# Optimization experiments

Measured on AMD Instinct MI355X. Metric: run time of the kernel, lower is better.

The kernel has to match this reference:

```python
import jax, jax.numpy as jnp
import numpy as np

B, S, H, E, K, D = 1, 4096, 1024, 8, 2, 2048

def setup_inputs() -> dict:
    key = jax.random.key(0)
    k1, k2, k3, k4, k5 = jax.random.split(key, 5)
    x = jax.random.normal(k1, (B, S, H), dtype=jnp.float32)
    attention_mask = jnp.ones((B, S), dtype=jnp.int32)
    expert_weights = jax.random.uniform(k2, (B, S, K), dtype=jnp.float32)
    # distinct top-K expert indices per token (torch code requires at most one match per token)
    r = jax.random.uniform(k3, (B, S, E))
    chosen_expert_indices = jnp.argsort(r, axis=-1)[..., :K].astype(jnp.int64)
    down_proj = jax.random.normal(k4, (E, H, D), dtype=jnp.float32)
    up_proj = jax.random.normal(k5, (E, D, H), dtype=jnp.float32)
    return {"x": x, "attention_mask": attention_mask, "expert_weights": expert_weights,
            "chosen_expert_indices": chosen_expert_indices, "down_proj": down_proj, "up_proj": up_proj}

def reference(x, attention_mask, expert_weights, chosen_expert_indices, down_proj, up_proj):
    b, s, h = x.shape
    e = down_proj.shape[0]
    xt = x.reshape(-1, h)                                   # [N,H]
    n = xt.shape[0]
    mask = attention_mask.reshape(n, 1).astype(x.dtype)     # [N,1]
    idx = chosen_expert_indices.reshape(n, -1)              # [N,K]
    w = expert_weights.reshape(n, -1)                       # [N,K]
    onehot = jax.nn.one_hot(idx, e, dtype=x.dtype)          # [N,K,E]
    # per-token routing weight for each expert (0 if not chosen), masked
    we = jnp.einsum('nk,nke->ne', w, onehot) * mask         # [N,E]
    hid = jax.nn.relu(jnp.einsum('nh,ehd->end', xt, down_proj))  # [E,N,D]
    y = jnp.einsum('end,edh->enh', hid, up_proj)            # [E,N,H]
    mlp = jnp.einsum('ne,enh->nh', we, y)                   # [N,H]
    out = xt + mlp                                          # residual (B==1 as in source)
    return out.reshape(b, s, h)
```

## Files before the change

### kernel.cpp

```cpp
#include <hip/hip_runtime.h>
#include <stdint.h>

#define NTOK 4096
#define HDIM 1024
#define DDIM 2048
#define NEXP 8
#define NASS 8192

typedef __attribute__((ext_vector_type(8))) short bf16x8;
typedef __attribute__((ext_vector_type(4))) float f32x4;

typedef __attribute__((address_space(1))) const unsigned int gu32;
typedef __attribute__((address_space(3))) unsigned int lu32;

#define BARRIER() asm volatile("s_barrier" ::: "memory")
#define WAIT_VM0() asm volatile("s_waitcnt vmcnt(0)" ::: "memory")
#define WAIT_LGKM0() do { asm volatile("s_waitcnt lgkmcnt(0)" ::: "memory"); \
                          __builtin_amdgcn_sched_barrier(0); } while (0)

__device__ __forceinline__ void async16(void* lds, const void* g) {
  __builtin_amdgcn_global_load_lds((gu32*)(uintptr_t)g, (lu32*)(uintptr_t)lds, 16, 0, 0);
}

__device__ __forceinline__ unsigned short f2bf(float f) {
  unsigned int u = __float_as_uint(f);
  return (unsigned short)((u + 0x7fffu + ((u >> 16) & 1u)) >> 16);
}
__device__ __forceinline__ float bf2f(unsigned short u) {
  return __uint_as_float(((unsigned int)u) << 16);
}

__global__ __launch_bounds__(256) void k_cvt_x(const float* __restrict__ x,
                                               unsigned short* __restrict__ x16) {
  int i = blockIdx.x * 256 + threadIdx.x;
  float4 v = reinterpret_cast<const float4*>(x)[i];
  ushort4 o;
  o.x = f2bf(v.x); o.y = f2bf(v.y); o.z = f2bf(v.z); o.w = f2bf(v.w);
  reinterpret_cast<ushort4*>(x16)[i] = o;
}

__global__ __launch_bounds__(256) void k_transpose(const float* __restrict__ in,
                                                   unsigned short* __restrict__ out,
                                                   int R, int C) {
  __shared__ float t[32][33];
  const size_t mbase = (size_t)blockIdx.z * R * C;
  int tid = threadIdx.x;
  int r = tid >> 3, c4 = (tid & 7) * 4;
  int gr = blockIdx.y * 32 + r;
  int gc = blockIdx.x * 32 + c4;
  float4 v = *reinterpret_cast<const float4*>(in + mbase + (size_t)gr * C + gc);
  t[r][c4 + 0] = v.x; t[r][c4 + 1] = v.y; t[r][c4 + 2] = v.z; t[r][c4 + 3] = v.w;
  __syncthreads();
  int orow = blockIdx.x * 32 + r;
  int oc4  = blockIdx.y * 32 + c4;
  ushort4 o;
  o.x = f2bf(t[c4 + 0][r]); o.y = f2bf(t[c4 + 1][r]);
  o.z = f2bf(t[c4 + 2][r]); o.w = f2bf(t[c4 + 3][r]);
  *reinterpret_cast<ushort4*>(out + mbase + (size_t)orow * R + oc4) = o;
}

__global__ __launch_bounds__(1024) void k_route(
    const int* __restrict__ idx, const float* __restrict__ ew,
    const int* __restrict__ amask,
    int* __restrict__ counts_g, int* __restrict__ offs_g,
    int* __restrict__ toks, float* __restrict__ wl, int* __restrict__ slotmap) {
  __shared__ int cnt[NEXP], cur[NEXP], flag;
  const int t = threadIdx.x;
  if (t < NEXP) cnt[t] = 0;
  if (t == 0) flag = 0;
  __syncthreads();
  int lf = 0;
#pragma unroll
  for (int j = 0; j < 4; ++j) {
    int i = t + j * 1024;
    if (idx[2 * i + 1] != 0) lf = 1;
  }
  if (lf) atomicOr(&flag, 1);
  __syncthreads();
  const int is32 = flag;
  int e[8];
#pragma unroll
  for (int j = 0; j < 8; ++j) {
    int i = t + j * 1024;
    int ei = is32 ? idx[i] : idx[2 * i];
    e[j] = ei;
    atomicAdd(&cnt[ei], 1);
  }
  __syncthreads();
  if (t == 0) {
    int off = 0;
    for (int k = 0; k < NEXP; ++k) {
      cur[k] = off; offs_g[k] = off; counts_g[k] = cnt[k]; off += cnt[k];
    }
  }
  __syncthreads();
#pragma unroll
  for (int j = 0; j < 8; ++j) {
    int i = t + j * 1024;
    int n = i >> 1;
    int slot = atomicAdd(&cur[e[j]], 1);
    toks[slot] = n;
    wl[slot] = ew[i] * (amask[n] ? 1.0f : 0.0f);
    slotmap[i] = slot;
  }
}

__global__ __launch_bounds__(512, 2) void k_gemm_down(
    const unsigned short* __restrict__ x16, const unsigned short* __restrict__ bT,
    const int* __restrict__ counts, const int* __restrict__ offs,
    const int* __restrict__ toks, unsigned short* __restrict__ hid) {
  const int e = blockIdx.x;
  const int cnt = counts[e];
  const int q = blockIdx.y;
  const int mt = q >> 3;
  const int nt = q & 7;
  if (mt * 256 >= cnt) return;
  const int base = offs[e];
  __shared__ alignas(16) char lds[131072];
  const int tid = threadIdx.x;
  const int lane = tid & 63;
  const int wr = ((tid >> 8) & 1) * 128;
  const int wc = ((tid >> 6) & 3) * 64;

  const char* gA[4]; const char* gB[4]; int sOff[4];
  {
    const int swcol = ((tid & 7) << 4) ^ (((tid >> 3) & 7) << 4);
#pragma unroll
    for (int s = 0; s < 4; ++s) {
      int row = s * 64 + (tid >> 3);
      int sl = mt * 256 + row; if (sl >= cnt) sl = cnt - 1;
      gA[s] = (const char*)(x16 + (size_t)toks[base + sl] * HDIM) + swcol;
      gB[s] = (const char*)(bT + (size_t)e * DDIM * HDIM + (size_t)(nt * 256 + row) * HDIM) + swcol;
      sOff[s] = s * 8192 + tid * 16;
    }
  }
  const int swz = (lane & 7) << 4;
  const int lo = (lane >> 4) << 4;
  int rowA[8], rowB[4];
#pragma unroll
  for (int m = 0; m < 8; ++m) rowA[m] = (wr + m * 16 + (lane & 15)) * 128;
#pragma unroll
  for (int n = 0; n < 4; ++n) rowB[n] = (wc + n * 16 + (lane & 15)) * 128;

#pragma unroll
  for (int s = 0; s < 4; ++s) {
    async16(lds + sOff[s], gA[s]);
    async16(lds + 65536 + sOff[s], gB[s]);
  }

  f32x4 acc[8][4] = {};
  for (int j = 0; j < 16; ++j) {
    WAIT_VM0();
    BARRIER();
    char* curA = lds + ((j & 1) << 15);
    char* curB = lds + 65536 + ((j & 1) << 15);
    if (j < 15) {
      const int ko = (j + 1) << 7;
      char* nA = lds + ((~j & 1) << 15);
      char* nB = lds + 65536 + ((~j & 1) << 15);
#pragma unroll
      for (int s = 0; s < 4; ++s) {
        async16(nA + sOff[s], gA[s] + ko);
        async16(nB + sOff[s], gB[s] + ko);
      }
    }
#pragma unroll
    for (int ks = 0; ks < 2; ++ks) {
      const int cx = ((ks << 6) | lo) ^ swz;
      bf16x8 fa[8], fb[4];
#pragma unroll
      for (int n = 0; n < 4; ++n) fb[n] = *reinterpret_cast<const bf16x8*>(curB + rowB[n] + cx);
#pragma unroll
      for (int m = 0; m < 8; ++m) fa[m] = *reinterpret_cast<const bf16x8*>(curA + rowA[m] + cx);
      WAIT_LGKM0();
      __builtin_amdgcn_s_setprio(1);
#pragma unroll
      for (int m = 0; m < 8; ++m)
#pragma unroll
        for (int n = 0; n < 4; ++n)
          acc[m][n] = __builtin_amdgcn_mfma_f32_16x16x32_bf16(fa[m], fb[n], acc[m][n], 0, 0, 0);
      __builtin_amdgcn_s_setprio(0);
    }
  }

#pragma unroll
  for (int m = 0; m < 8; ++m) {
    int r0 = mt * 256 + wr + m * 16 + ((lane >> 4) * 4);
#pragma unroll
    for (int jj = 0; jj < 4; ++jj) {
      int r = r0 + jj;
      if (r < cnt) {
        unsigned short* dst = hid + (size_t)(base + r) * DDIM + nt * 256 + wc + (lane & 15);
#pragma unroll
        for (int n = 0; n < 4; ++n) {
          float v = acc[m][n][jj];
          dst[n * 16] = f2bf(v > 0.f ? v : 0.f);
        }
      }
    }
  }
}

__global__ __launch_bounds__(512, 2) void k_gemm_up(
    const unsigned short* __restrict__ hid, const unsigned short* __restrict__ bT,
    const int* __restrict__ counts, const int* __restrict__ offs,
    unsigned short* __restrict__ yw) {
  const int e = blockIdx.x;
  const int cnt = counts[e];
  const int q = blockIdx.y;
  const int nt = q & 3;
  const int mt = (q >> 2) & 15;
  const int ksp = q >> 6;
  if (mt * 256 >= cnt) return;
  const int base = offs[e];
  __shared__ alignas(16) char lds[131072];
  const int tid = threadIdx.x;
  const int lane = tid & 63;
  const int wr = ((tid >> 8) & 1) * 128;
  const int wc = ((tid >> 6) & 3) * 64;

  const char* gA[4]; const char* gB[4]; int sOff[4];
  {
    const int swcol = ((tid & 7) << 4) ^ (((tid >> 3) & 7) << 4);
#pragma unroll
    for (int s = 0; s < 4; ++s) {
      int row = s * 64 + (tid >> 3);
      int sl = mt * 256 + row; if (sl >= cnt) sl = cnt - 1;
      gA[s] = (const char*)(hid + (size_t)(base + sl) * DDIM + ksp * 1024) + swcol;
      gB[s] = (const char*)(bT + (size_t)e * HDIM * DDIM + (size_t)(nt * 256 + row) * DDIM + ksp * 1024) + swcol;
      sOff[s] = s * 8192 + tid * 16;
    }
  }
  const int swz = (lane & 7) << 4;
  const int lo = (lane >> 4) << 4;
  int rowA[8], rowB[4];
#pragma unroll
  for (int m = 0; m < 8; ++m) rowA[m] = (wr + m * 16 + (lane & 15)) * 128;
#pragma unroll
  for (int n = 0; n < 4; ++n) rowB[n] = (wc + n * 16 + (lane & 15)) * 128;

#pragma unroll
  for (int s = 0; s < 4; ++s) {
    async16(lds + sOff[s], gA[s]);
    async16(lds + 65536 + sOff[s], gB[s]);
  }

  f32x4 acc[8][4] = {};
  for (int j = 0; j < 16; ++j) {
    WAIT_VM0();
    BARRIER();
    char* curA = lds + ((j & 1) << 15);
    char* curB = lds + 65536 + ((j & 1) << 15);
    if (j < 15) {
      const int ko = (j + 1) << 7;
      char* nA = lds + ((~j & 1) << 15);
      char* nB = lds + 65536 + ((~j & 1) << 15);
#pragma unroll
      for (int s = 0; s < 4; ++s) {
        async16(nA + sOff[s], gA[s] + ko);
        async16(nB + sOff[s], gB[s] + ko);
      }
    }
#pragma unroll
    for (int ks = 0; ks < 2; ++ks) {
      const int cx = ((ks << 6) | lo) ^ swz;
      bf16x8 fa[8], fb[4];
#pragma unroll
      for (int n = 0; n < 4; ++n) fb[n] = *reinterpret_cast<const bf16x8*>(curB + rowB[n] + cx);
#pragma unroll
      for (int m = 0; m < 8; ++m) fa[m] = *reinterpret_cast<const bf16x8*>(curA + rowA[m] + cx);
      WAIT_LGKM0();
      __builtin_amdgcn_s_setprio(1);
#pragma unroll
      for (int m = 0; m < 8; ++m)
#pragma unroll
        for (int n = 0; n < 4; ++n)
          acc[m][n] = __builtin_amdgcn_mfma_f32_16x16x32_bf16(fa[m], fb[n], acc[m][n], 0, 0, 0);
      __builtin_amdgcn_s_setprio(0);
    }
  }

#pragma unroll
  for (int m = 0; m < 8; ++m) {
    int r0 = mt * 256 + wr + m * 16 + ((lane >> 4) * 4);
#pragma unroll
    for (int jj = 0; jj < 4; ++jj) {
      int r = r0 + jj;
      if (r < cnt) {
        unsigned short* dst = yw + ((size_t)ksp * NASS + base + r) * HDIM
                              + nt * 256 + wc + (lane & 15);
#pragma unroll
        for (int n = 0; n < 4; ++n) dst[n * 16] = f2bf(acc[m][n][jj]);
      }
    }
  }
}

__global__ __launch_bounds__(256) void k_combine(
    const float* __restrict__ x, const unsigned short* __restrict__ yw,
    const int* __restrict__ slotmap, const float* __restrict__ wl,
    float* __restrict__ out) {
  const int n = blockIdx.x;
  const int t = threadIdx.x;
  const int s0 = slotmap[2 * n], s1 = slotmap[2 * n + 1];
  const float w0 = wl[s0], w1 = wl[s1];
  float4 xv = reinterpret_cast<const float4*>(x + (size_t)n * HDIM)[t];
  ushort4 a0 = reinterpret_cast<const ushort4*>(yw + (size_t)s0 * HDIM)[t];
  ushort4 a1 = reinterpret_cast<const ushort4*>(yw + ((size_t)NASS + s0) * HDIM)[t];
  ushort4 b0 = reinterpret_cast<const ushort4*>(yw + (size_t)s1 * HDIM)[t];
  ushort4 b1 = reinterpret_cast<const ushort4*>(yw + ((size_t)NASS + s1) * HDIM)[t];
  float4 r;
  r.x = xv.x + w0 * (bf2f(a0.x) + bf2f(a1.x)) + w1 * (bf2f(b0.x) + bf2f(b1.x));
  r.y = xv.y + w0 * (bf2f(a0.y) + bf2f(a1.y)) + w1 * (bf2f(b0.y) + bf2f(b1.y));
  r.z = xv.z + w0 * (bf2f(a0.z) + bf2f(a1.z)) + w1 * (bf2f(b0.z) + bf2f(b1.z));
  r.w = xv.w + w0 * (bf2f(a0.w) + bf2f(a1.w)) + w1 * (bf2f(b0.w) + bf2f(b1.w));
  reinterpret_cast<float4*>(out + (size_t)n * HDIM)[t] = r;
}

extern "C" void kernel_launch(void* const* d_in, const int* in_sizes, int n_in,
                              void* d_out, int out_size, void* d_ws, size_t ws_size,
                              hipStream_t stream) {
  const float* x    = (const float*)d_in[0];
  const int* amask  = (const int*)d_in[1];
  const float* ew   = (const float*)d_in[2];
  const int* cidx   = (const int*)d_in[3];
  const float* dn   = (const float*)d_in[4];
  const float* up   = (const float*)d_in[5];
  float* out        = (float*)d_out;
  char* ws          = (char*)d_ws;

  const size_t X16_OFF = 0;
  const size_t DNT_OFF = X16_OFF + (size_t)NTOK * HDIM * 2;
  const size_t UPT_OFF = DNT_OFF + (size_t)NEXP * HDIM * DDIM * 2;
  const size_t HID_OFF = UPT_OFF + (size_t)NEXP * HDIM * DDIM * 2;
  const size_t MET_OFF = HID_OFF + (size_t)NASS * DDIM * 2;

  unsigned short* x16 = (unsigned short*)(ws + X16_OFF);
  unsigned short* dnT = (unsigned short*)(ws + DNT_OFF);
  unsigned short* upT = (unsigned short*)(ws + UPT_OFF);
  unsigned short* hid = (unsigned short*)(ws + HID_OFF);
  unsigned short* yw  = (unsigned short*)(ws + DNT_OFF);
  int* counts  = (int*)(ws + MET_OFF);
  int* offs    = counts + 8;
  int* toks    = counts + 32;
  float* wl    = (float*)(toks + NASS);
  int* slotmap = (int*)(wl + NASS);

  k_cvt_x<<<NTOK * HDIM / 1024, 256, 0, stream>>>(x, x16);
  k_transpose<<<dim3(DDIM / 32, HDIM / 32, NEXP), 256, 0, stream>>>(dn, dnT, HDIM, DDIM);
  k_transpose<<<dim3(HDIM / 32, DDIM / 32, NEXP), 256, 0, stream>>>(up, upT, DDIM, HDIM);
  k_route<<<1, 1024, 0, stream>>>(cidx, ew, amask, counts, offs, toks, wl, slotmap);
  k_gemm_down<<<dim3(8, 128), 512, 0, stream>>>(x16, dnT, counts, offs, toks, hid);
  k_gemm_up<<<dim3(8, 128), 512, 0, stream>>>(hid, upT, counts, offs, yw);
  k_combine<<<NTOK, 256, 0, stream>>>(x, yw, slotmap, wl, out);
}
```

Measured before the change: 172.2 us.

## Fuse prep kernels, shrink GEMM tiles to 128x128, drop up-proj split-K

Merges the x conversion and both weight transposes into one prep launch. Both grouped GEMMs go from 256x256 tiles with 512 threads to 128x128 tiles with 256 threads and half the LDS, so more blocks can be resident per CU. The up GEMM no longer splits K into two partial outputs, so the combine step reads one partial per expert instead of two. Smaller tiles lower per-block operand reuse and raise total global traffic for the weights.

```diff
diff --git a/kernel.cpp b/kernel.cpp
--- a/kernel.cpp
+++ b/kernel.cpp
@@ -30,33 +30,50 @@
   return __uint_as_float(((unsigned int)u) << 16);
 }
 
-__global__ __launch_bounds__(256) void k_cvt_x(const float* __restrict__ x,
-                                               unsigned short* __restrict__ x16) {
-  int i = blockIdx.x * 256 + threadIdx.x;
-  float4 v = reinterpret_cast<const float4*>(x)[i];
+__device__ __forceinline__ void transpose_tile(const float* __restrict__ in,
+                                               unsigned short* __restrict__ out,
+                                               int R, int C, int e, int bx, int by,
+                                               float* tb, int tid) {
+  const size_t mbase = (size_t)e * R * C;
+  int r = tid >> 3, c4 = (tid & 7) * 4;
+  int gr = by * 32 + r;
+  int gc = bx * 32 + c4;
+  float4 v = *reinterpret_cast<const float4*>(in + mbase + (size_t)gr * C + gc);
+  tb[r * 33 + c4 + 0] = v.x; tb[r * 33 + c4 + 1] = v.y;
+  tb[r * 33 + c4 + 2] = v.z; tb[r * 33 + c4 + 3] = v.w;
+  __syncthreads();
+  int orow = bx * 32 + r;
+  int oc4  = by * 32 + c4;
   ushort4 o;
-  o.x = f2bf(v.x); o.y = f2bf(v.y); o.z = f2bf(v.z); o.w = f2bf(v.w);
-  reinterpret_cast<ushort4*>(x16)[i] = o;
-}
-
-__global__ __launch_bounds__(256) void k_transpose(const float* __restrict__ in,
-                                                   unsigned short* __restrict__ out,
-                                                   int R, int C) {
-  __shared__ float t[32][33];
-  const size_t mbase = (size_t)blockIdx.z * R * C;
-  int tid = threadIdx.x;
-  int r = tid >> 3, c4 = (tid & 7) * 4;
-  int gr = blockIdx.y * 32 + r;
-  int gc = blockIdx.x * 32 + c4;
-  float4 v = *reinterpret_cast<const float4*>(in + mbase + (size_t)gr * C + gc);
-  t[r][c4 + 0] = v.x; t[r][c4 + 1] = v.y; t[r][c4 + 2] = v.z; t[r][c4 + 3] = v.w;
-  __syncthreads();
-  int orow = blockIdx.x * 32 + r;
-  int oc4  = blockIdx.y * 32 + c4;
-  ushort4 o;
-  o.x = f2bf(t[c4 + 0][r]); o.y = f2bf(t[c4 + 1][r]);
-  o.z = f2bf(t[c4 + 2][r]); o.w = f2bf(t[c4 + 3][r]);
+  o.x = f2bf(tb[(c4 + 0) * 33 + r]); o.y = f2bf(tb[(c4 + 1) * 33 + r]);
+  o.z = f2bf(tb[(c4 + 2) * 33 + r]); o.w = f2bf(tb[(c4 + 3) * 33 + r]);
   *reinterpret_cast<ushort4*>(out + mbase + (size_t)orow * R + oc4) = o;
+}
+
+__global__ __launch_bounds__(256) void k_prep(
+    const float* __restrict__ x, unsigned short* __restrict__ x16,
+    const float* __restrict__ dn, unsigned short* __restrict__ dnT,
+    const float* __restrict__ up, unsigned short* __restrict__ upT) {
+  __shared__ float tb[32 * 33];
+  const int b = blockIdx.x;
+  const int tid = threadIdx.x;
+  if (b < 4096) {
+    int i = b * 256 + tid;
+    float4 v = reinterpret_cast<const float4*>(x)[i];
+    ushort4 o;
+    o.x = f2bf(v.x); o.y = f2bf(v.y); o.z = f2bf(v.z); o.w = f2bf(v.w);
+    reinterpret_cast<ushort4*>(x16)[i] = o;
+  } else if (b < 4096 + 16384) {
+    int idx = b - 4096;
+    int e = idx >> 11, t = idx & 2047;
+    int bx = t & 63, by = t >> 6;
+    transpose_tile(dn, dnT, HDIM, DDIM, e, bx, by, tb, tid);
+  } else {
+    int idx = b - 20480;
+    int e = idx >> 11, t = idx & 2047;
+    int bx = t & 31, by = t >> 5;
+    transpose_tile(up, upT, DDIM, HDIM, e, bx, by, tb, tid);
+  }
 }
 
 __global__ __launch_bounds__(1024) void k_route(
@@ -105,59 +122,59 @@
   }
 }
 
-__global__ __launch_bounds__(512, 2) void k_gemm_down(
+__global__ __launch_bounds__(256, 4) void k_gemm_down(
     const unsigned short* __restrict__ x16, const unsigned short* __restrict__ bT,
     const int* __restrict__ counts, const int* __restrict__ offs,
     const int* __restrict__ toks, unsigned short* __restrict__ hid) {
   const int e = blockIdx.x;
   const int cnt = counts[e];
   const int q = blockIdx.y;
-  const int mt = q >> 3;
-  const int nt = q & 7;
-  if (mt * 256 >= cnt) return;
+  const int mt = q >> 4;
+  const int nt = q & 15;
+  if (mt * 128 >= cnt) return;
   const int base = offs[e];
-  __shared__ alignas(16) char lds[131072];
+  __shared__ alignas(16) char lds[65536];
   const int tid = threadIdx.x;
   const int lane = tid & 63;
-  const int wr = ((tid >> 8) & 1) * 128;
-  const int wc = ((tid >> 6) & 3) * 64;
+  const int wr = ((tid >> 7) & 1) * 64;
+  const int wc = ((tid >> 6) & 1) * 64;
 
   const char* gA[4]; const char* gB[4]; int sOff[4];
   {
     const int swcol = ((tid & 7) << 4) ^ (((tid >> 3) & 7) << 4);
 #pragma unroll
     for (int s = 0; s < 4; ++s) {
-      int row = s * 64 + (tid >> 3);
-      int sl = mt * 256 + row; if (sl >= cnt) sl = cnt - 1;
+      int row = s * 32 + (tid >> 3);
+      int sl = mt * 128 + row; if (sl >= cnt) sl = cnt - 1;
       gA[s] = (const char*)(x16 + (size_t)toks[base + sl] * HDIM) + swcol;
-      gB[s] = (const char*)(bT + (size_t)e * DDIM * HDIM + (size_t)(nt * 256 + row) * HDIM) + swcol;
-      sOff[s] = s * 8192 + tid * 16;
+      gB[s] = (const char*)(bT + (size_t)e * DDIM * HDIM + (size_t)(nt * 128 + row) * HDIM) + swcol;
+      sOff[s] = s * 4096 + tid * 16;
     }
   }
   const int swz = (lane & 7) << 4;
   const int lo = (lane >> 4) << 4;
-  int rowA[8], rowB[4];
-#pragma unroll
-  for (int m = 0; m < 8; ++m) rowA[m] = (wr + m * 16 + (lane & 15)) * 128;
+  int rowA[4], rowB[4];
+#pragma unroll
+  for (int m = 0; m < 4; ++m) rowA[m] = (wr + m * 16 + (lane & 15)) * 128;
 #pragma unroll
   for (int n = 0; n < 4; ++n) rowB[n] = (wc + n * 16 + (lane & 15)) * 128;
 
 #pragma unroll
   for (int s = 0; s < 4; ++s) {
     async16(lds + sOff[s], gA[s]);
-    async16(lds + 65536 + sOff[s], gB[s]);
-  }
-
-  f32x4 acc[8][4] = {};
+    async16(lds + 32768 + sOff[s], gB[s]);
+  }
+
+  f32x4 acc[4][4] = {};
   for (int j = 0; j < 16; ++j) {
     WAIT_VM0();
     BARRIER();
-    char* curA = lds + ((j & 1) << 15);
-    char* curB = lds + 65536 + ((j & 1) << 15);
+    char* curA = lds + ((j & 1) << 14);
+    char* curB = lds + 32768 + ((j & 1) << 14);
     if (j < 15) {
       const int ko = (j + 1) << 7;
-      char* nA = lds + ((~j & 1) << 15);
-      char* nB = lds + 65536 + ((~j & 1) << 15);
+      char* nA = lds + ((~j & 1) << 14);
+      char* nB = lds + 32768 + ((~j & 1) << 14);
 #pragma unroll
       for (int s = 0; s < 4; ++s) {
         async16(nA + sOff[s], gA[s] + ko);
@@ -167,15 +184,15 @@
 #pragma unroll
     for (int ks = 0; ks < 2; ++ks) {
       const int cx = ((ks << 6) | lo) ^ swz;
-      bf16x8 fa[8], fb[4];
+      bf16x8 fa[4], fb[4];
 #pragma unroll
       for (int n = 0; n < 4; ++n) fb[n] = *reinterpret_cast<const bf16x8*>(curB + rowB[n] + cx);
 #pragma unroll
-      for (int m = 0; m < 8; ++m) fa[m] = *reinterpret_cast<const bf16x8*>(curA + rowA[m] + cx);
+      for (int m = 0; m < 4; ++m) fa[m] = *reinterpret_cast<const bf16x8*>(curA + rowA[m] + cx);
       WAIT_LGKM0();
       __builtin_amdgcn_s_setprio(1);
 #pragma unroll
-      for (int m = 0; m < 8; ++m)
+      for (int m = 0; m < 4; ++m)
 #pragma unroll
         for (int n = 0; n < 4; ++n)
           acc[m][n] = __builtin_amdgcn_mfma_f32_16x16x32_bf16(fa[m], fb[n], acc[m][n], 0, 0, 0);
@@ -184,13 +201,13 @@
   }
 
 #pragma unroll
-  for (int m = 0; m < 8; ++m) {
-    int r0 = mt * 256 + wr + m * 16 + ((lane >> 4) * 4);
+  for (int m = 0; m < 4; ++m) {
+    int r0 = mt * 128 + wr + m * 16 + ((lane >> 4) * 4);
 #pragma unroll
     for (int jj = 0; jj < 4; ++jj) {
       int r = r0 + jj;
       if (r < cnt) {
-        unsigned short* dst = hid + (size_t)(base + r) * DDIM + nt * 256 + wc + (lane & 15);
+        unsigned short* dst = hid + (size_t)(base + r) * DDIM + nt * 128 + wc + (lane & 15);
 #pragma unroll
         for (int n = 0; n < 4; ++n) {
           float v = acc[m][n][jj];
@@ -201,60 +218,59 @@
   }
 }
 
-__global__ __launch_bounds__(512, 2) void k_gemm_up(
+__global__ __launch_bounds__(256, 4) void k_gemm_up(
     const unsigned short* __restrict__ hid, const unsigned short* __restrict__ bT,
     const int* __restrict__ counts, const int* __restrict__ offs,
     unsigned short* __restrict__ yw) {
   const int e = blockIdx.x;
   const int cnt = counts[e];
   const int q = blockIdx.y;
-  const int nt = q & 3;
-  const int mt = (q >> 2) & 15;
-  const int ksp = q >> 6;
-  if (mt * 256 >= cnt) return;
+  const int mt = q >> 3;
+  const int nt = q & 7;
+  if (mt * 128 >= cnt) return;
   const int base = offs[e];
-  __shared__ alignas(16) char lds[131072];
+  __shared__ alignas(16) char lds[65536];
   const int tid = threadIdx.x;
   const int lane = tid & 63;
-  const int wr = ((tid >> 8) & 1) * 128;
-  const int wc = ((tid >> 6) & 3) * 64;
+  const int wr = ((tid >> 7) & 1) * 64;
+  const int wc = ((tid >> 6) & 1) * 64;
 
   const char* gA[4]; const char* gB[4]; int sOff[4];
   {
     const int swcol = ((tid & 7) << 4) ^ (((tid >> 3) & 7) << 4);
 #pragma unroll
     for (int s = 0; s < 4; ++s) {
-      int row = s * 64 + (tid >> 3);
-      int sl = mt * 256 + row; if (sl >= cnt) sl = cnt - 1;
-      gA[s] = (const char*)(hid + (size_t)(base + sl) * DDIM + ksp * 1024) + swcol;
-      gB[s] = (const char*)(bT + (size_t)e * HDIM * DDIM + (size_t)(nt * 256 + row) * DDIM + ksp * 1024) + swcol;
-      sOff[s] = s * 8192 + tid * 16;
+      int row = s * 32 + (tid >> 3);
+      int sl = mt * 128 + row; if (sl >= cnt) sl = cnt - 1;
+      gA[s] = (const char*)(hid + (size_t)(base + sl) * DDIM) + swcol;
+      gB[s] = (const char*)(bT + (size_t)e * HDIM * DDIM + (size_t)(nt * 128 + row) * DDIM) + swcol;
+      sOff[s] = s * 4096 + tid * 16;
     }
   }
   const int swz = (lane & 7) << 4;
   const int lo = (lane >> 4) << 4;
-  int rowA[8], rowB[4];
-#pragma unroll
-  for (int m = 0; m < 8; ++m) rowA[m] = (wr + m * 16 + (lane & 15)) * 128;
+  int rowA[4], rowB[4];
+#pragma unroll
+  for (int m = 0; m < 4; ++m) rowA[m] = (wr + m * 16 + (lane & 15)) * 128;
 #pragma unroll
   for (int n = 0; n < 4; ++n) rowB[n] = (wc + n * 16 + (lane & 15)) * 128;
 
 #pragma unroll
   for (int s = 0; s < 4; ++s) {
     async16(lds + sOff[s], gA[s]);
-    async16(lds + 65536 + sOff[s], gB[s]);
-  }
-
-  f32x4 acc[8][4] = {};
-  for (int j = 0; j < 16; ++j) {
+    async16(lds + 32768 + sOff[s], gB[s]);
+  }
+
+  f32x4 acc[4][4] = {};
+  for (int j = 0; j < 32; ++j) {
     WAIT_VM0();
     BARRIER();
-    char* curA = lds + ((j & 1) << 15);
-    char* curB = lds + 65536 + ((j & 1) << 15);
-    if (j < 15) {
+    char* curA = lds + ((j & 1) << 14);
+    char* curB = lds + 32768 + ((j & 1) << 14);
+    if (j < 31) {
       const int ko = (j + 1) << 7;
-      char* nA = lds + ((~j & 1) << 15);
-      char* nB = lds + 65536 + ((~j & 1) << 15);
+      char* nA = lds + ((~j & 1) << 14);
+      char* nB = lds + 32768 + ((~j & 1) << 14);
 #pragma unroll
       for (int s = 0; s < 4; ++s) {
         async16(nA + sOff[s], gA[s] + ko);
@@ -264,15 +280,15 @@
 #pragma unroll
     for (int ks = 0; ks < 2; ++ks) {
       const int cx = ((ks << 6) | lo) ^ swz;
-      bf16x8 fa[8], fb[4];
+      bf16x8 fa[4], fb[4];
 #pragma unroll
       for (int n = 0; n < 4; ++n) fb[n] = *reinterpret_cast<const bf16x8*>(curB + rowB[n] + cx);
 #pragma unroll
-      for (int m = 0; m < 8; ++m) fa[m] = *reinterpret_cast<const bf16x8*>(curA + rowA[m] + cx);
+      for (int m = 0; m < 4; ++m) fa[m] = *reinterpret_cast<const bf16x8*>(curA + rowA[m] + cx);
       WAIT_LGKM0();
       __builtin_amdgcn_s_setprio(1);
 #pragma unroll
-      for (int m = 0; m < 8; ++m)
+      for (int m = 0; m < 4; ++m)
 #pragma unroll
         for (int n = 0; n < 4; ++n)
           acc[m][n] = __builtin_amdgcn_mfma_f32_16x16x32_bf16(fa[m], fb[n], acc[m][n], 0, 0, 0);
@@ -281,14 +297,13 @@
   }
 
 #pragma unroll
-  for (int m = 0; m < 8; ++m) {
-    int r0 = mt * 256 + wr + m * 16 + ((lane >> 4) * 4);
+  for (int m = 0; m < 4; ++m) {
+    int r0 = mt * 128 + wr + m * 16 + ((lane >> 4) * 4);
 #pragma unroll
     for (int jj = 0; jj < 4; ++jj) {
       int r = r0 + jj;
       if (r < cnt) {
-        unsigned short* dst = yw + ((size_t)ksp * NASS + base + r) * HDIM
-                              + nt * 256 + wc + (lane & 15);
+        unsigned short* dst = yw + (size_t)(base + r) * HDIM + nt * 128 + wc + (lane & 15);
 #pragma unroll
         for (int n = 0; n < 4; ++n) dst[n * 16] = f2bf(acc[m][n][jj]);
       }
@@ -306,14 +321,12 @@
   const float w0 = wl[s0], w1 = wl[s1];
   float4 xv = reinterpret_cast<const float4*>(x + (size_t)n * HDIM)[t];
   ushort4 a0 = reinterpret_cast<const ushort4*>(yw + (size_t)s0 * HDIM)[t];
-  ushort4 a1 = reinterpret_cast<const ushort4*>(yw + ((size_t)NASS + s0) * HDIM)[t];
   ushort4 b0 = reinterpret_cast<const ushort4*>(yw + (size_t)s1 * HDIM)[t];
-  ushort4 b1 = reinterpret_cast<const ushort4*>(yw + ((size_t)NASS + s1) * HDIM)[t];
   float4 r;
-  r.x = xv.x + w0 * (bf2f(a0.x) + bf2f(a1.x)) + w1 * (bf2f(b0.x) + bf2f(b1.x));
-  r.y = xv.y + w0 * (bf2f(a0.y) + bf2f(a1.y)) + w1 * (bf2f(b0.y) + bf2f(b1.y));
-  r.z = xv.z + w0 * (bf2f(a0.z) + bf2f(a1.z)) + w1 * (bf2f(b0.z) + bf2f(b1.z));
-  r.w = xv.w + w0 * (bf2f(a0.w) + bf2f(a1.w)) + w1 * (bf2f(b0.w) + bf2f(b1.w));
+  r.x = xv.x + w0 * bf2f(a0.x) + w1 * bf2f(b0.x);
+  r.y = xv.y + w0 * bf2f(a0.y) + w1 * bf2f(b0.y);
+  r.z = xv.z + w0 * bf2f(a0.z) + w1 * bf2f(b0.z);
+  r.w = xv.w + w0 * bf2f(a0.w) + w1 * bf2f(b0.w);
   reinterpret_cast<float4*>(out + (size_t)n * HDIM)[t] = r;
 }
 
@@ -346,11 +359,9 @@
   float* wl    = (float*)(toks + NASS);
   int* slotmap = (int*)(wl + NASS);
 
-  k_cvt_x<<<NTOK * HDIM / 1024, 256, 0, stream>>>(x, x16);
-  k_transpose<<<dim3(DDIM / 32, HDIM / 32, NEXP), 256, 0, stream>>>(dn, dnT, HDIM, DDIM);
-  k_transpose<<<dim3(HDIM / 32, DDIM / 32, NEXP), 256, 0, stream>>>(up, upT, DDIM, HDIM);
+  k_prep<<<4096 + 16384 + 16384, 256, 0, stream>>>(x, x16, dn, dnT, up, upT);
   k_route<<<1, 1024, 0, stream>>>(cidx, ew, amask, counts, offs, toks, wl, slotmap);
-  k_gemm_down<<<dim3(8, 128), 512, 0, stream>>>(x16, dnT, counts, offs, toks, hid);
-  k_gemm_up<<<dim3(8, 128), 512, 0, stream>>>(hid, upT, counts, offs, yw);
+  k_gemm_down<<<dim3(8, 1024), 256, 0, stream>>>(x16, dnT, counts, offs, toks, hid);
+  k_gemm_up<<<dim3(8, 512), 256, 0, stream>>>(hid, upT, counts, offs, yw);
   k_combine<<<NTOK, 256, 0, stream>>>(x, yw, slotmap, wl, out);
 }
```

Result: faster. 156.5 us (-9.1%).
